# Kernel optimization log

Hardware: AMD Instinct MI355X
Metric: run time of the kernel (lower is better)

The kernel has to match this reference:

```python
import jax, jax.numpy as jnp
import numpy as np

E = 255  # embedding_dim (complete d-ary tree size)
D = 2    # tree degree; parent(i) = (i-1)//D


def _tree_levels(embeddim, d):
    """Precompute (child_idx, parent_idx) per tree level, deepest first.

    Level-wise processing is equivalent to the original serial loop
    i = embeddim-1 .. 1: m[..., (i-1)//d] += m[..., i], because children
    always have larger indices than parents and nodes within one level
    are never ancestors of each other.
    """
    depth = np.zeros(embeddim, dtype=np.int64)
    for i in range(1, embeddim):
        depth[i] = depth[(i - 1) // d] + 1
    levels = []
    for lv in range(int(depth.max()), 0, -1):
        idx = np.nonzero(depth == lv)[0]
        levels.append((jnp.asarray(idx), jnp.asarray((idx - 1) // d)))
    return levels

_LEVELS = _tree_levels(E, D)


def tree_subtree_sum(m):
    # Bottom-up subtree cumulative sum over the last axis (Tree_ops.forward).
    for child, parent in _LEVELS:
        m = m.at[..., parent].add(m[..., child])  # duplicate parents accumulate
    return m


def setup_inputs() -> dict:
    key = jax.random.key(0)
    k1, k2, k3 = jax.random.split(key, 3)
    num_emb = 100000
    batch, n = 4096, 50
    x = jax.random.randint(k1, (batch, n), 0, num_emb)
    y = jax.random.randint(k2, (batch, n), 0, num_emb)
    # init: uniform(-1,1) rows scaled to radius 0.001 (as in __init__)
    r = jax.random.uniform(k3, (num_emb, E), minval=-1.0, maxval=1.0, dtype=jnp.float32)
    emb = 0.001 * r / jnp.linalg.norm(r, axis=-1, keepdims=True)
    weight = jnp.ones((E,), dtype=jnp.float32)
    return {"x": x, "y": y, "emb": emb, "weight": weight}


def reference(x, y, emb, weight):
    # TreeWE scoring: softmax over tree-node probs, subtree-sum, weighted L1.
    xp = jax.nn.softmax(emb[x], axis=2)   # [B, N, E]
    yp = jax.nn.softmax(emb[y], axis=2)
    xs = tree_subtree_sum(xp)
    ys = tree_subtree_sum(yp)
    # torch.norm(., p=1, dim=2) == sum of abs over last axis
    return -jnp.sum(jnp.abs((xs - ys) * weight), axis=2)  # [B, N]
```

## Files before the change

### kernel.cpp

```cpp
#include <hip/hip_runtime.h>

#define EDIM 255
#define EPAD 256

__device__ __forceinline__ float wave_reduce_sum(float v) {
    #pragma unroll
    for (int off = 32; off > 0; off >>= 1) v += __shfl_xor(v, off, 64);
    return v;
}
__device__ __forceinline__ float wave_reduce_max(float v) {
    #pragma unroll
    for (int off = 32; off > 0; off >>= 1) v = fmaxf(v, __shfl_xor(v, off, 64));
    return v;
}

__global__ __launch_bounds__(256) void row_transform_b_kernel(
    const float* __restrict__ emb, const float* __restrict__ w,
    unsigned short* __restrict__ tq, int n_rows)
{
    __shared__ float sm[4][EPAD];
    const int lane = threadIdx.x & 63;
    const int wv   = threadIdx.x >> 6;
    const int r    = blockIdx.x * 4 + wv;
    const bool active = r < n_rows;

    float wreg[4], base[4];
    #pragma unroll
    for (int j = 0; j < 4; ++j) {
        const int e = 64 * j + lane;
        if (e < EDIM) {
            wreg[j] = w[e];
            const int lvl = 31 - __clz(e + 1);
            base[j] = (float)((256 >> lvl) - 1) * (1.0f / 255.0f);
        } else { wreg[j] = 0.f; base[j] = 0.f; }
    }

    if (active) {
        const float* row = emb + (size_t)r * EDIM;
        float v[4];
        #pragma unroll
        for (int j = 0; j < 4; ++j) {
            const int e = 64 * j + lane;
            v[j] = (e < EDIM) ? row[e] : -1e30f;
        }
        float s = 0.f;
        #pragma unroll
        for (int j = 0; j < 4; ++j) { v[j] = __expf(v[j]); s += v[j]; }
        s = wave_reduce_sum(s);
        const float is = 1.0f / s;
        #pragma unroll
        for (int j = 0; j < 4; ++j) sm[wv][64 * j + lane] = v[j] * is;
    }
    __syncthreads();

    #pragma unroll
    for (int cnt = 64; cnt >= 1; cnt >>= 1) {
        if (active && lane < cnt) {
            const int q = (cnt - 1) + lane;
            sm[wv][q] += sm[wv][2 * q + 1] + sm[wv][2 * q + 2];
        }
        __syncthreads();
    }

    if (active) {
        unsigned pk0 = 0, pk1 = 0;
        #pragma unroll
        for (int j = 0; j < 4; ++j) {
            const int e = 64 * j + lane;
            const float d = (sm[wv][e] - base[j]) * wreg[j];
            unsigned u = __float_as_uint(d);
            u += 0x7fffu + ((u >> 16) & 1u);
            const unsigned h = u >> 16;
            if (j == 0) pk0 = h;
            else if (j == 1) pk0 |= h << 16;
            else if (j == 2) pk1 = h;
            else pk1 |= h << 16;
        }
        uint2 pk; pk.x = pk0; pk.y = pk1;
        ((uint2*)(tq + (size_t)r * EPAD))[lane] = pk;
    }
}

__global__ __launch_bounds__(256) void pair_score_b_kernel(
    const int* __restrict__ x, const int* __restrict__ y,
    const unsigned short* __restrict__ tq, float* __restrict__ out, int n_pairs)
{
    const int lane   = threadIdx.x & 63;
    const int wv     = threadIdx.x >> 6;
    const int nwaves = gridDim.x * 4;

    int p = blockIdx.x * 4 + wv;
    if (p >= n_pairs) return;

    uint2 va = ((const uint2*)(tq + (size_t)x[p] * EPAD))[lane];
    uint2 vb = ((const uint2*)(tq + (size_t)y[p] * EPAD))[lane];

    while (true) {
        const int  pn   = p + nwaves;
        const bool more = pn < n_pairs;
        uint2 van = make_uint2(0u, 0u), vbn = van;
        if (more) {
            van = ((const uint2*)(tq + (size_t)x[pn] * EPAD))[lane];
            vbn = ((const uint2*)(tq + (size_t)y[pn] * EPAD))[lane];
        }

        const float a0 = __uint_as_float(va.x << 16);
        const float a1 = __uint_as_float(va.x & 0xffff0000u);
        const float a2 = __uint_as_float(va.y << 16);
        const float a3 = __uint_as_float(va.y & 0xffff0000u);
        const float b0 = __uint_as_float(vb.x << 16);
        const float b1 = __uint_as_float(vb.x & 0xffff0000u);
        const float b2 = __uint_as_float(vb.y << 16);
        const float b3 = __uint_as_float(vb.y & 0xffff0000u);
        float s = fabsf(a0 - b0) + fabsf(a1 - b1)
                + fabsf(a2 - b2) + fabsf(a3 - b3);
        s = wave_reduce_sum(s);
        if (lane == 0) out[p] = -s;

        if (!more) break;
        p = pn; va = van; vb = vbn;
    }
}

__global__ __launch_bounds__(256) void treewe_score_kernel(
    const int* __restrict__ x, const int* __restrict__ y,
    const float* __restrict__ emb, const float* __restrict__ w,
    float* __restrict__ out, int n_pairs)
{
    __shared__ float sm[4][EPAD];
    const int lane = threadIdx.x & 63;
    const int wv   = threadIdx.x >> 6;
    const int p    = blockIdx.x * 4 + wv;
    const bool active = p < n_pairs;

    if (active) {
        const float* rowx = emb + (size_t)x[p] * EDIM;
        const float* rowy = emb + (size_t)y[p] * EDIM;
        float vx[4], vy[4];
        #pragma unroll
        for (int j = 0; j < 4; ++j) {
            const int e = 64 * j + lane;
            const bool in = (e < EDIM);
            vx[j] = in ? rowx[e] : -1e30f;
            vy[j] = in ? rowy[e] : -1e30f;
        }
        float mx = wave_reduce_max(fmaxf(fmaxf(vx[0], vx[1]), fmaxf(vx[2], vx[3])));
        float ex[4], sx = 0.f;
        #pragma unroll
        for (int j = 0; j < 4; ++j) { ex[j] = __expf(vx[j] - mx); sx += ex[j]; }
        sx = wave_reduce_sum(sx);
        float my = wave_reduce_max(fmaxf(fmaxf(vy[0], vy[1]), fmaxf(vy[2], vy[3])));
        float ey[4], sy = 0.f;
        #pragma unroll
        for (int j = 0; j < 4; ++j) { ey[j] = __expf(vy[j] - my); sy += ey[j]; }
        sy = wave_reduce_sum(sy);
        const float ixs = 1.0f / sx, iys = 1.0f / sy;
        #pragma unroll
        for (int j = 0; j < 4; ++j)
            sm[wv][64 * j + lane] = ex[j] * ixs - ey[j] * iys;
    }
    __syncthreads();
    #pragma unroll
    for (int cnt = 64; cnt >= 1; cnt >>= 1) {
        if (active && lane < cnt) {
            const int q = (cnt - 1) + lane;
            sm[wv][q] += sm[wv][2 * q + 1] + sm[wv][2 * q + 2];
        }
        __syncthreads();
    }
    float part = 0.f;
    if (active) {
        #pragma unroll
        for (int j = 0; j < 4; ++j) {
            const int e = 64 * j + lane;
            if (e < EDIM) part += fabsf(sm[wv][e] * w[e]);
        }
    }
    part = wave_reduce_sum(part);
    if (active && lane == 0) out[p] = -part;
}

extern "C" void kernel_launch(void* const* d_in, const int* in_sizes, int n_in,
                              void* d_out, int out_size, void* d_ws, size_t ws_size,
                              hipStream_t stream) {
    const int*   x   = (const int*)d_in[0];
    const int*   y   = (const int*)d_in[1];
    const float* emb = (const float*)d_in[2];
    const float* w   = (const float*)d_in[3];
    float* out = (float*)d_out;

    const int n_pairs = in_sizes[0];
    const int n_rows  = in_sizes[2] / EDIM;

    const size_t need = (size_t)n_rows * EPAD * sizeof(unsigned short);
    if (ws_size >= need) {
        unsigned short* tq = (unsigned short*)d_ws;
        const int g1 = (n_rows + 3) / 4;
        const int g2 = min(2048, (n_pairs + 3) / 4);
        row_transform_b_kernel<<<g1, 256, 0, stream>>>(emb, w, tq, n_rows);
        pair_score_b_kernel<<<g2, 256, 0, stream>>>(x, y, tq, out, n_pairs);
    } else {
        treewe_score_kernel<<<(n_pairs + 3) / 4, 256, 0, stream>>>(
            x, y, emb, w, out, n_pairs);
    }
}
```

Before: 70.28 us.

## Persist row-transform waves with prefetch and barrier-free per-wave tree reduction

Turns the row transform kernel into a grid-stride persistent loop capped at 2048 blocks. Each wave prefetches the next embedding row while it processes the current one. The block-wide __syncthreads between tree levels are replaced with per-wave LDS waitcnt fences, since each wave owns its own LDS row. The top tree levels now use shuffles, and children are read with float2 loads through a shifted index. This targets barrier stalls and launch/tail overhead over 100k rows, at the cost of relying on wave-local LDS ordering assumptions.

```diff
diff --git a/kernel.cpp b/kernel.cpp
--- a/kernel.cpp
+++ b/kernel.cpp
@@ -2,6 +2,11 @@
 
 #define EDIM 255
 #define EPAD 256
+
+#define LDS_FENCE() do { \
+    asm volatile("s_waitcnt lgkmcnt(0)" ::: "memory"); \
+    __builtin_amdgcn_sched_barrier(0); \
+} while (0)
 
 __device__ __forceinline__ float wave_reduce_sum(float v) {
     #pragma unroll
@@ -18,11 +23,11 @@
     const float* __restrict__ emb, const float* __restrict__ w,
     unsigned short* __restrict__ tq, int n_rows)
 {
-    __shared__ float sm[4][EPAD];
-    const int lane = threadIdx.x & 63;
-    const int wv   = threadIdx.x >> 6;
-    const int r    = blockIdx.x * 4 + wv;
-    const bool active = r < n_rows;
+    __shared__ __align__(16) float sm[4][264];
+    const int lane   = threadIdx.x & 63;
+    const int wv     = threadIdx.x >> 6;
+    const int nwaves = gridDim.x * 4;
+    float* Q = sm[wv];
 
     float wreg[4], base[4];
     #pragma unroll
@@ -35,39 +40,66 @@
         } else { wreg[j] = 0.f; base[j] = 0.f; }
     }
 
-    if (active) {
+    int r = blockIdx.x * 4 + wv;
+    if (r >= n_rows) return;
+
+    float v[4];
+    {
         const float* row = emb + (size_t)r * EDIM;
-        float v[4];
         #pragma unroll
         for (int j = 0; j < 4; ++j) {
             const int e = 64 * j + lane;
             v[j] = (e < EDIM) ? row[e] : -1e30f;
         }
-        float s = 0.f;
-        #pragma unroll
-        for (int j = 0; j < 4; ++j) { v[j] = __expf(v[j]); s += v[j]; }
+    }
+
+    while (true) {
+        const int  rn   = r + nwaves;
+        const bool more = rn < n_rows;
+        float vn[4];
+        if (more) {
+            const float* rown = emb + (size_t)rn * EDIM;
+            #pragma unroll
+            for (int j = 0; j < 4; ++j) {
+                const int e = 64 * j + lane;
+                vn[j] = (e < EDIM) ? rown[e] : -1e30f;
+            }
+        }
+
+        float pexp[4], s = 0.f;
+        #pragma unroll
+        for (int j = 0; j < 4; ++j) { pexp[j] = __expf(v[j]); s += pexp[j]; }
         s = wave_reduce_sum(s);
         const float is = 1.0f / s;
         #pragma unroll
-        for (int j = 0; j < 4; ++j) sm[wv][64 * j + lane] = v[j] * is;
-    }
-    __syncthreads();
-
-    #pragma unroll
-    for (int cnt = 64; cnt >= 1; cnt >>= 1) {
-        if (active && lane < cnt) {
-            const int q = (cnt - 1) + lane;
-            sm[wv][q] += sm[wv][2 * q + 1] + sm[wv][2 * q + 2];
-        }
-        __syncthreads();
-    }
-
-    if (active) {
+        for (int j = 0; j < 4; ++j) Q[1 + 64 * j + lane] = pexp[j] * is;
+        LDS_FENCE();
+
+        #pragma unroll
+        for (int cnt = 64; cnt >= 8; cnt >>= 1) {
+            if (lane < cnt) {
+                const int q = (cnt - 1) + lane;
+                const float2 c = *(const float2*)&Q[2 * q + 2];
+                Q[q + 1] += c.x + c.y;
+            }
+            LDS_FENCE();
+        }
+
+        float t = Q[8 + (lane >> 3)];
+        t = Q[4 + (lane >> 4)] + t + __shfl_xor(t, 8, 64);
+        const float t2 = t;
+        t = Q[2 + (lane >> 5)] + t + __shfl_xor(t, 16, 64);
+        const float t1 = t;
+        t = Q[1] + t + __shfl_xor(t, 32, 64);
+        if (!(lane & 15)) Q[4 + (lane >> 4)] = t2;
+        if (!(lane & 31)) Q[2 + (lane >> 5)] = t1;
+        if (lane == 0)    Q[1] = t;
+        LDS_FENCE();
+
         unsigned pk0 = 0, pk1 = 0;
         #pragma unroll
         for (int j = 0; j < 4; ++j) {
-            const int e = 64 * j + lane;
-            const float d = (sm[wv][e] - base[j]) * wreg[j];
+            const float d = (Q[1 + 64 * j + lane] - base[j]) * wreg[j];
             unsigned u = __float_as_uint(d);
             u += 0x7fffu + ((u >> 16) & 1u);
             const unsigned h = u >> 16;
@@ -78,6 +110,11 @@
         }
         uint2 pk; pk.x = pk0; pk.y = pk1;
         ((uint2*)(tq + (size_t)r * EPAD))[lane] = pk;
+
+        if (!more) break;
+        r = rn;
+        #pragma unroll
+        for (int j = 0; j < 4; ++j) v[j] = vn[j];
     }
 }
 
@@ -195,7 +232,7 @@
     const size_t need = (size_t)n_rows * EPAD * sizeof(unsigned short);
     if (ws_size >= need) {
         unsigned short* tq = (unsigned short*)d_ws;
-        const int g1 = (n_rows + 3) / 4;
+        const int g1 = min(2048, (n_rows + 3) / 4);
         const int g2 = min(2048, (n_pairs + 3) / 4);
         row_transform_b_kernel<<<g1, 256, 0, stream>>>(emb, w, tq, n_rows);
         pair_score_b_kernel<<<g2, 256, 0, stream>>>(x, y, tq, out, n_pairs);
```

Result: no change. 71.23 us (+1.4%).
